# Optimization experiments

Measured on AMD Instinct MI355X. Metric: run time of the kernel, lower is better.

Reference implementation:

```python
import jax, jax.numpy as jnp
import numpy as np

N, E_SC, E_BB = 50000, 600000, 100000
D, ED, REMB, NRES, SBF = 128, 128, 32, 21, 16
PI = 3.14159


def ln(x, g, b):
    m = jnp.mean(x, -1, keepdims=True)
    v = jnp.mean((x - m) ** 2, -1, keepdims=True)
    return (x - m) * jax.lax.rsqrt(v + 1e-5) * g + b


def gcn(x, W, b, src, dst, w):
    # GCNConv: symmetric normalization with unit self-loops and edge weights w.
    n = x.shape[0]
    xw = x @ W
    deg = jax.ops.segment_sum(w, dst, num_segments=n) + 1.0  # +1 self-loop
    dis = jax.lax.rsqrt(jnp.maximum(deg, 1e-6))  # clamp: hat_e.mean can be negative
    norm = dis[src] * w * dis[dst]
    agg = jax.ops.segment_sum(norm[:, None] * xw[src], dst, num_segments=n)
    return agg + (dis * dis)[:, None] * xw + b


def core(V_com, SBF_chi, X_c_alpha, V_c_beta, SBF_phi, SBF_psi, d_sidechain_com, d_min,
         old_chi, old_phi, old_psi, old_cbeta_coords, old_calpha_coords,
         res_table, sc_ln_g, sc_ln_b, sc_W, sc_b, bb_ln_g, bb_ln_b, bb_W, bb_b,
         e_ln_g, e_ln_b, eW1, eb1, eW2, eb2, euW, eub, gW, gb, bgW, bgb,
         iW1, ib1, iW2, ib2, aW, ab, baW, bab, cW, cb, xW, xb,
         residue_idx_i, residue_idx_j, edge_index_sc, edge_index_bb):
    hat_h = ln(jnp.concatenate([V_com, SBF_chi], -1), sc_ln_g, sc_ln_b) @ sc_W + sc_b
    h = ln(jnp.concatenate([X_c_alpha, V_c_beta, SBF_phi, SBF_psi], -1), bb_ln_g, bb_ln_b) @ bb_W + bb_b
    pair = jnp.concatenate([res_table[residue_idx_i], res_table[residue_idx_j]], -1)
    e_in = jnp.concatenate([d_sidechain_com[:, None], d_min[:, None], pair], -1)
    hat_e = jax.nn.relu(ln(e_in, e_ln_g, e_ln_b) @ eW1 + eb1) @ eW2 + eb2
    src, dst = edge_index_sc[0], edge_index_sc[1]
    for _ in range(3):  # num_sidechain_layers
        w = hat_e.mean(-1)
        hat_h = hat_h + jax.nn.relu(gcn(hat_h, gW, gb, src, dst, w))
        hat_e = hat_e + jnp.concatenate([hat_h[src], hat_h[dst]], -1) @ euW + eub
    bsrc, bdst = edge_index_bb[0], edge_index_bb[1]
    ebb = jnp.ones(bsrc.shape[0], hat_h.dtype)
    for _ in range(2):
        m = jax.nn.relu(jnp.concatenate([h, hat_h], -1) @ iW1 + ib1) @ iW2 + ib2
        h = h + jax.nn.relu(gcn(h, bgW, bgb, bsrc, bdst, ebb)) + m
    sc_act = jax.nn.relu(hat_h)
    bb_act = jax.nn.relu(h)
    wrap = lambda a: (a + PI) % (2.0 * PI) - PI
    dchi = (sc_act @ aW + ab)[:, 0]
    chi_new = wrap(old_chi + dchi[None, :])  # [4, N]
    dphi = (bb_act @ baW + bab)[:, 0]
    phi_new = wrap(old_phi + dphi)
    psi_new = wrap(old_psi + dphi)  # same bb_angle_head applied twice in source
    V_cbeta_new = old_cbeta_coords + sc_act @ cW + cb
    X_calpha_new = old_calpha_coords + bb_act @ xW + xb
    return chi_new, phi_new, psi_new, V_cbeta_new, X_calpha_new


def setup_inputs() -> dict:
    key = jax.random.key(0)
    ks = jax.random.split(key, 40)
    rn = lambda i, s: jax.random.normal(ks[i], s, jnp.float32)
    p = lambda i, s: rn(i, s) * 0.05
    return dict(
        V_com=rn(0, (N, 3)), SBF_chi=rn(1, (N, SBF)), X_c_alpha=rn(2, (N, 3)),
        V_c_beta=rn(3, (N, 3)), SBF_phi=rn(4, (N, SBF)), SBF_psi=rn(5, (N, SBF)),
        d_sidechain_com=jax.random.uniform(ks[6], (E_SC,), jnp.float32),
        d_min=jax.random.uniform(ks[7], (E_SC,), jnp.float32),
        old_chi=rn(8, (4, N)), old_phi=rn(9, (N,)), old_psi=rn(10, (N,)),
        old_cbeta_coords=rn(11, (N, 3)), old_calpha_coords=rn(12, (N, 3)),
        res_table=p(13, (NRES, REMB)),
        sc_ln_g=jnp.ones(3 + SBF), sc_ln_b=jnp.zeros(3 + SBF), sc_W=p(14, (3 + SBF, D)), sc_b=jnp.zeros(D),
        bb_ln_g=jnp.ones(6 + 2 * SBF), bb_ln_b=jnp.zeros(6 + 2 * SBF), bb_W=p(15, (6 + 2 * SBF, D)), bb_b=jnp.zeros(D),
        e_ln_g=jnp.ones(2 + 2 * REMB), e_ln_b=jnp.zeros(2 + 2 * REMB),
        eW1=p(16, (2 + 2 * REMB, ED)), eb1=jnp.zeros(ED), eW2=p(17, (ED, ED)), eb2=jnp.zeros(ED),
        euW=p(18, (2 * D, ED)), eub=jnp.zeros(ED),
        gW=p(19, (D, D)), gb=jnp.zeros(D), bgW=p(20, (D, D)), bgb=jnp.zeros(D),
        iW1=p(21, (2 * D, D)), ib1=jnp.zeros(D), iW2=p(22, (D, D)), ib2=jnp.zeros(D),
        aW=p(23, (D, 1)), ab=jnp.zeros(1), baW=p(24, (D, 1)), bab=jnp.zeros(1),
        cW=p(25, (D, 3)), cb=jnp.zeros(3), xW=p(26, (D, 3)), xb=jnp.zeros(3),
        residue_idx_i=jax.random.randint(ks[27], (E_SC,), 0, NRES),
        residue_idx_j=jax.random.randint(ks[28], (E_SC,), 0, NRES),
        edge_index_sc=jax.random.randint(ks[29], (2, E_SC), 0, N),
        edge_index_bb=jax.random.randint(ks[30], (2, E_BB), 0, N),
    )


def reference(V_com, SBF_chi, X_c_alpha, V_c_beta, SBF_phi, SBF_psi, d_sidechain_com, d_min,
              old_chi, old_phi, old_psi, old_cbeta_coords, old_calpha_coords,
              res_table, sc_ln_g, sc_ln_b, sc_W, sc_b, bb_ln_g, bb_ln_b, bb_W, bb_b,
              e_ln_g, e_ln_b, eW1, eb1, eW2, eb2, euW, eub, gW, gb, bgW, bgb,
              iW1, ib1, iW2, ib2, aW, ab, baW, bab, cW, cb, xW, xb,
              residue_idx_i, residue_idx_j, edge_index_sc, edge_index_bb):
    return core(V_com, SBF_chi, X_c_alpha, V_c_beta, SBF_phi, SBF_psi, d_sidechain_com, d_min,
                old_chi, old_phi, old_psi, old_cbeta_coords, old_calpha_coords,
                res_table, sc_ln_g, sc_ln_b, sc_W, sc_b, bb_ln_g, bb_ln_b, bb_W, bb_b,
                e_ln_g, e_ln_b, eW1, eb1, eW2, eb2, euW, eub, gW, gb, bgW, bgb,
                iW1, ib1, iW2, ib2, aW, ab, baW, bab, cW, cb, xW, xb,
                residue_idx_i, residue_idx_j, edge_index_sc, edge_index_bb)
```

## Files before the change

### kernel.cpp

```cpp
#include <hip/hip_runtime.h>
#include <stdint.h>

#define DEVI __device__ __forceinline__

constexpr int N_   = 50000;
constexpr int ESC  = 600000;
constexpr int EBB  = 100000;
constexpr int NRES = 21;
constexpr float PI_F = 3.14159f;

constexpr int RCH = 2048;
constexpr int RBS = (ESC + RCH - 1)/RCH;
constexpr int RBB = (EBB + RCH - 1)/RCH;

typedef __attribute__((ext_vector_type(8))) short short8v;
typedef __attribute__((ext_vector_type(4))) float f32x4;

DEVI float bf2f(unsigned short u){ return __uint_as_float(((unsigned)u)<<16); }
DEVI unsigned short f2bf(float f){
  unsigned x = __float_as_uint(f);
  unsigned r = (x + 0x7FFFu + ((x>>16)&1u))>>16;
  return (unsigned short)r;
}
DEVI float ldin(const void* p, long i, int f32){
// ... 196 lines not shown
  int NB = g? RBB : RBS;
  int* H = hist + (g? (long)RBS*256 : 0);
  int t=threadIdx.x;
  int i0=t, i1=t+256;
  int o0 = (i0<NB)? H[(long)i0*256+d] : 0;
  int o1 = (i1<NB)? H[(long)i1*256+d] : 0;
  sA[i0]=o0; sA[i1]=o1;
  __syncthreads();
  int* a=sA; int* b=sB;
  for(int off=1; off<512; off<<=1){
    b[i0] = a[i0] + ((i0>=off)? a[i0-off]:0);
    b[i1] = a[i1] + ((i1>=off)? a[i1-off]:0);
    __syncthreads();
    int* tmp=a; a=b; b=tmp;
  }
  if(i0<NB) H[(long)i0*256+d] = a[i0]-o0;
  if(i1<NB) H[(long)i1*256+d] = a[i1]-o1;
  if(t==255) tot[(g?256:0)+d] = a[511];
}
__global__ void k_rscanB(const int* tot, int* base){
  __shared__ int sA[256], sB[256];
  int t=threadIdx.x;
  for(int g=0;g<2;g++){
    int o=tot[g*256+t];
    sA[t]=o; __syncthreads();
    int* a=sA; int* b=sB;
    for(int off=1; off<256; off<<=1){
      b[t] = a[t] + ((t>=off)? a[t-off]:0);
      __syncthreads();
      int* tmp=a; a=b; b=tmp;
    }
    base[g*256+t] = a[t]-o;
    __syncthreads();
  }
}
__global__ void k_rscat(int shift, int first,
    const int* kin_sc, const int* srcv_sc, const int2* pin_sc,
    const int* kin_bb, const int* srcv_bb, const int2* pin_bb,
    const int* hist, const int* dbase,
    int* kout_sc, int2* pout_sc, int* kout_bb, int2* pout_bb){
  __shared__ int running[256];
  __shared__ int Hb[256];
  __shared__ int whist[4][256];
  __shared__ int pw[4][256];
  int tid=threadIdx.x, lane=tid&63, w=tid>>6;
  int g = blockIdx.x>=RBS;
  const int* kin  = g? kin_bb : kin_sc;
  const int* srcv = g? srcv_bb: srcv_sc;
  const int2* pin = g? pin_bb : pin_sc;
  int* kout  = g? kout_bb : kout_sc;
  int2* pout = g? pout_bb : pout_sc;
  int E = g? EBB : ESC;
  int b = g? blockIdx.x-RBS : blockIdx.x;
  running[tid]=0;
  Hb[tid]=hist[(long)blockIdx.x*256+tid] + dbase[(g?256:0)+tid];
  int base=b*RCH;
  for(int r=0;r<RCH/256;r++){
    __syncthreads();
    whist[0][tid]=0; whist[1][tid]=0; whist[2][tid]=0; whist[3][tid]=0;
    __syncthreads();
    int idx=base+r*256+tid;
    bool valid = idx<E;
    int key=0, digit=0; int2 pay; pay.x=0; pay.y=0;
    if(valid){
      key=kin[idx];
      digit=(key>>shift)&255;
      if(first){ pay.x=srcv[idx]; pay.y=idx; }
      else pay=pin[idx];
    }
    unsigned long long act=__ballot(valid);
    unsigned long long same=act;
    #pragma unroll
    for(int k=0;k<8;k++){
      unsigned long long m=__ballot(valid && ((digit>>k)&1));
      same &= ((digit>>k)&1)? m : ~m;
    }
    same &= act;
    unsigned long long below=(1ULL<<lane)-1ULL;
    int wrank=__popcll(same & below);
    if(valid && wrank==0) whist[w][digit]=__popcll(same);
    __syncthreads();
    int c0=whist[0][tid], c1=whist[1][tid], c2=whist[2][tid], c3=whist[3][tid];
    pw[0][tid]=0; pw[1][tid]=c0; pw[2][tid]=c0+c1; pw[3][tid]=c0+c1+c2;
    __syncthreads();
    if(valid){
      int pos=Hb[digit]+running[digit]+pw[w][digit]+wrank;
      kout[pos]=key; pout[pos]=pay;
    }
    __syncthreads();
    running[tid]+=c0+c1+c2+c3;
  }
}
__global__ void k_bounds(const int* dstS_sc, const int* dstS_bb, int* rp_sc, int* rp_bb){
  long i=(long)blockIdx.x*blockDim.x+threadIdx.x;
  if(i<=ESC){
    int cur = (i<ESC)? dstS_sc[i] : N_;
    int prev= (i>0)? dstS_sc[i-1] : -1;
    for(int d=prev+1; d<=cur; d++) rp_sc[d]=(int)i;
  } else if(i <= (long)ESC+1+EBB){
    long j=i-(ESC+1);
    int cur = (j<EBB)? dstS_bb[j] : N_;
    int prev= (j>0)? dstS_bb[j-1] : -1;
    for(int d=prev+1; d<=cur; d++) rp_bb[d]=(int)j;
  }
}
__global__ void k_degb(const int* rp, float* disb){
  int n=blockIdx.x*blockDim.x+threadIdx.x;
  if(n<N_) disb[n]=rsqrtf(1.f+(float)(rp[n+1]-rp[n]));
}

constexpr int WBG = (ESC + 63)/64;
__global__ __launch_bounds__(256,4) void k_w0(const void* dsc, const void* dmin,
    const int* ri_, const int* rj_, const int* flag, const float* dvf,
    const float* P, const float* sp, const float* qp, float* we){
  int wv=threadIdx.x>>6, lane=threadIdx.x&63;
  int g=lane>>4, l=lane&15;
  long ebase=(long)blockIdx.x*64 + wv*16 + g*4;
  int f32=*flag;
  int j0=l*8;
  float4 A0=*(const float4*)&dvf[j0],     A1=*(const float4*)&dvf[j0+4];
  float4 C0=*(const float4*)&dvf[128+j0], C1=*(const float4*)&dvf[128+j0+4];
  float4 G0=*(const float4*)&dvf[256+j0], G1=*(const float4*)&dvf[256+j0+4];
  float4 B0=*(const float4*)&dvf[384+j0], B1=*(const float4*)&dvf[384+j0+4];
  float4 V0=*(const float4*)&dvf[512+j0], V1=*(const float4*)&dvf[512+j0+4];
  float eb2=dvf[640];
  #pragma unroll
  for(int k=0;k<4;k++){
    long e=ebase+k;
    bool val = e<ESC;
    long ee = val? e : 0;
    float d1=ldin(dsc,ee,f32), d2=ldin(dmin,ee,f32);
    int c=ri_[ee]*NRES+rj_[ee];
    float m=(d1+d2+sp[c])*(1.f/66.f);
    float ms=(d1*d1+d2*d2+qp[c])*(1.f/66.f);
    float istd=rsqrtf(fmaxf(ms-m*m,0.f)+1e-5f);
    float nmi=-m*istd;
    float4 P0=*(const float4*)&P[(long)c*128+j0];
    float4 P1=*(const float4*)&P[(long)c*128+j0+4];
    float acc=0.f, t, hid;
    t=fmaf(d1,A0.x,fmaf(d2,C0.x,P0.x)); hid=fmaf(istd,t,fmaf(nmi,G0.x,B0.x)); acc=fmaf(fmaxf(hid,0.f),V0.x,acc);
    t=fmaf(d1,A0.y,fmaf(d2,C0.y,P0.y)); hid=fmaf(istd,t,fmaf(nmi,G0.y,B0.y)); acc=fmaf(fmaxf(hid,0.f),V0.y,acc);
    t=fmaf(d1,A0.z,fmaf(d2,C0.z,P0.z)); hid=fmaf(istd,t,fmaf(nmi,G0.z,B0.z)); acc=fmaf(fmaxf(hid,0.f),V0.z,acc);
    t=fmaf(d1,A0.w,fmaf(d2,C0.w,P0.w)); hid=fmaf(istd,t,fmaf(nmi,G0.w,B0.w)); acc=fmaf(fmaxf(hid,0.f),V0.w,acc);
    t=fmaf(d1,A1.x,fmaf(d2,C1.x,P1.x)); hid=fmaf(istd,t,fmaf(nmi,G1.x,B1.x)); acc=fmaf(fmaxf(hid,0.f),V1.x,acc);
    t=fmaf(d1,A1.y,fmaf(d2,C1.y,P1.y)); hid=fmaf(istd,t,fmaf(nmi,G1.y,B1.y)); acc=fmaf(fmaxf(hid,0.f),V1.y,acc);
    t=fmaf(d1,A1.z,fmaf(d2,C1.z,P1.z)); hid=fmaf(istd,t,fmaf(nmi,G1.z,B1.z)); acc=fmaf(fmaxf(hid,0.f),V1.z,acc);
    t=fmaf(d1,A1.w,fmaf(d2,C1.w,P1.w)); hid=fmaf(istd,t,fmaf(nmi,G1.w,B1.w)); acc=fmaf(fmaxf(hid,0.f),V1.w,acc);
    #pragma unroll
    for(int msk=1;msk<16;msk<<=1) acc+=__shfl_xor(acc,msk,64);
    if(l==0 && val) we[e]=acc+eb2;
  }
}

__global__ void k_deg(const int* rp, const int2* se, const float* we_edge,
                      const float* an, const float* bn, const float* dv,
                      float* we_csr, float* dis, int layer){
  int n=blockIdx.x*blockDim.x+threadIdx.x;
  if(n>=N_) return;
  int e0=rp[n], e1=rp[n+1];
  float s=1.f;
  if(layer==0){
    for(int p=e0;p<e1;p++){ float ww=we_edge[se[p].y]; we_csr[p]=ww; s+=ww; }
  } else {
    float add_n = bn[n] + dv[897];
    for(int p=e0;p<e1;p++){
      float ww=we_csr[p] + an[se[p].x] + add_n;
      we_csr[p]=ww; s+=ww;
    }
  }
  dis[n]=rsqrtf(fmaxf(s,1e-6f));
}
__global__ void k_norm(const int2* se, const float* we_csr, const float* dis, float* wn){
  int p=blockIdx.x*blockDim.x+threadIdx.x;
  if(p<ESC) wn[p]=dis[se[p].x]*we_csr[p];
}

DEVI f32x4 MFMA(short8v a, short8v b, f32x4 c){
  return __builtin_amdgcn_mfma_f32_16x16x32_bf16(a,b,c,0,0,0);
}
DEVI void cvt8(float4 a0, float4 a1, short8v& hi, short8v& lo){
  float av[8]={a0.x,a0.y,a0.z,a0.w,a1.x,a1.y,a1.z,a1.w};
  union{short8v v; unsigned short u[8];} H,L;
  #pragma unroll
  for(int i=0;i<8;i++){
    unsigned short h=f2bf(av[i]);
    float r=av[i]-bf2f(h);
    H.u[i]=h; L.u[i]=f2bf(r);
  }
  hi=H.v; lo=L.v;
}
DEVI short8v cvt8hi(float4 a0, float4 a1){
  union{short8v v; unsigned short u[8];} H;
  H.u[0]=f2bf(a0.x); H.u[1]=f2bf(a0.y); H.u[2]=f2bf(a0.z); H.u[3]=f2bf(a0.w);
  H.u[4]=f2bf(a1.x); H.u[5]=f2bf(a1.y); H.u[6]=f2bf(a1.z); H.u[7]=f2bf(a1.w);
  return H.v;
}

template<int KT, int LDA>
DEVI void mgemm_body(int bid, const float* A1, const float* A2,
    const unsigned short* Whi, const unsigned short* Wlo,
    const float* bias, float* C, int relu, int accum, int M){
  const int lane = threadIdx.x & 63;
  const int wid  = threadIdx.x >> 6;
  const int r0   = bid*64 + wid*16;
  const int mrow = lane & 15;
  const int kg   = lane >> 4;
  long arow = (long)min(r0 + mrow, M-1);
  f32x4 acc[8];
  #pragma unroll
  for(int t=0;t<8;t++) acc[t]=(f32x4){0.f,0.f,0.f,0.f};

  #pragma unroll
  for(int kt=0; kt<KT; kt++){
    const float* A = (KT==8 && kt>=4) ? A2 : A1;
    int kb = (kt&3)*32 + kg*8;
    float4 a0 = *(const float4*)&A[arow*LDA + kb];
    float4 a1 = *(const float4*)&A[arow*LDA + kb + 4];
    short8v ah, al; cvt8(a0,a1,ah,al);
    #pragma unroll
    for(int nt=0;nt<8;nt++){
      long off = (((long)kt*8+nt)*64 + lane)*8;
      short8v wh = *(const short8v*)&Whi[off];
      short8v wl = *(const short8v*)&Wlo[off];
      acc[nt] = MFMA(ah, wh, acc[nt]);
      acc[nt] = MFMA(al, wh, acc[nt]);
      acc[nt] = MFMA(ah, wl, acc[nt]);
      acc[nt] = MFMA(al, wl, acc[nt]);
    }
  }

  #pragma unroll
  for(int nt=0;nt<8;nt++){
    int col = nt*16 + mrow;
    float bj = bias ? bias[col] : 0.f;
    #pragma unroll
    for(int r=0;r<4;r++){
      int row = r0 + kg*4 + r;
      if(row >= M) continue;
      long idx = (long)row*128 + col;
      float v = acc[nt][r] + bj;
      if(relu) v = fmaxf(v,0.f);
      if(accum) v += C[idx];
      C[idx] = v;
    }
  }
}

template<int KT, int LDA>
__global__ __launch_bounds__(256,4) void k_mgemm(const float* A1, const float* A2,
    const unsigned short* Whi, const unsigned short* Wlo,
    const float* bias, float* C, int relu, int accum, int M){
  mgemm_body<KT,LDA>(blockIdx.x, A1, A2, Whi, Wlo, bias, C, relu, accum, M);
}

__global__ __launch_bounds__(256,4) void k_mfeat(const float* xn_sc, const float* xn_bb,
    const unsigned short* schi, const unsigned short* sclo,
    const unsigned short* bbhi, const unsigned short* bblo,
    const float* w, float* hat_h, float* hbuf, int M){
  int GBl=(M+63)/64;
  if((int)blockIdx.x < GBl)
    mgemm_body<1,32>(blockIdx.x, xn_sc, nullptr, schi, sclo, w+OW_SC_B, hat_h, 0,0,M);
  else
    mgemm_body<2,64>(blockIdx.x-GBl, xn_bb, nullptr, bbhi, bblo, w+OW_BB_B, hbuf, 0,0,M);
}

__global__ __launch_bounds__(256,4) void k_mbb(const float* h, const float* hh,
    const unsigned short* W1hi,
    const unsigned short* W2hi,
    const unsigned short* W3hi,
    const float* b1, const float* b2,
    unsigned short* xwout, unsigned short* mout, int M){
  __shared__ unsigned short hids[64*136];
  const int lane = threadIdx.x & 63;
  const int wid  = threadIdx.x >> 6;
  const int r0   = blockIdx.x*64 + wid*16;
  const int mrow = lane & 15;
  const int kg   = lane >> 4;
  long arow = (long)min(r0 + mrow, M-1);
  f32x4 acc1[8], acc2[8];
  #pragma unroll
  for(int t=0;t<8;t++){ acc1[t]=(f32x4){0,0,0,0}; acc2[t]=(f32x4){0,0,0,0}; }

  #pragma unroll
  for(int kt=0; kt<8; kt++){
    const float* A = (kt>=4) ? hh : h;
    int kb = (kt&3)*32 + kg*8;
    float4 a0 = *(const float4*)&A[arow*128 + kb];
    float4 a1 = *(const float4*)&A[arow*128 + kb + 4];
    short8v ah = cvt8hi(a0,a1);
    #pragma unroll
    for(int nt=0;nt<8;nt++){
      long off = (((long)kt*8+nt)*64 + lane)*8;
      acc1[nt] = MFMA(ah, *(const short8v*)&W1hi[off], acc1[nt]);
    }
    if(kt<4){
      #pragma unroll
      for(int nt=0;nt<8;nt++){
        long off = (((long)kt*8+nt)*64 + lane)*8;
        acc2[nt] = MFMA(ah, *(const short8v*)&W2hi[off], acc2[nt]);
      }
    }
  }

  #pragma unroll
  for(int nt=0;nt<8;nt++){
    int col = nt*16 + mrow;
    float bj = b1[col];
    #pragma unroll
    for(int r=0;r<4;r++){
      int rloc = wid*16 + kg*4 + r;
      int row = r0 + kg*4 + r;
      hids[rloc*136 + col] = f2bf(fmaxf(acc1[nt][r] + bj, 0.f));
      if(row < M) xwout[(long)row*128 + col] = f2bf(acc2[nt][r]);
    }
  }
  __syncthreads();

  f32x4 acc3[8];
  #pragma unroll
  for(int t=0;t<8;t++) acc3[t]=(f32x4){0,0,0,0};
  int rloc = wid*16 + mrow;
  #pragma unroll
  for(int kt=0; kt<4; kt++){
    int kb = kt*32 + kg*8;
    short8v ah = *(const short8v*)&hids[rloc*136 + kb];
    #pragma unroll
    for(int nt=0;nt<8;nt++){
      long off = (((long)kt*8+nt)*64 + lane)*8;
      acc3[nt] = MFMA(ah, *(const short8v*)&W3hi[off], acc3[nt]);
    }
  }
  #pragma unroll
  for(int nt=0;nt<8;nt++){
    int col = nt*16 + mrow;
    float bj = b2[col];
    #pragma unroll
    for(int r=0;r<4;r++){
      int row = r0 + kg*4 + r;
      if(row < M) mout[(long)row*128 + col] = f2bf(acc3[nt][r] + bj);
    }
  }
}

__global__ void k_agg_sc(const int* rp, const int2* se, const float* wn,
                         const float* dis, const float* xw, const float* w,
                         float* hat_h, const float* dv, float* an, float* bn, int withdot){
  int wv=threadIdx.x>>6, lane=threadIdx.x&63;
  int n=blockIdx.x*4+wv;
  int g=lane>>4, l=lane&15, d0=l*8;
  float disn=dis[n];
  float4 aA={0,0,0,0}, aB={0,0,0,0}, cA={0,0,0,0}, cB={0,0,0,0};
  int e0=rp[n], e1=rp[n+1];
  int p=e0+g;
  for(; p+4<e1; p+=8){
    int s0=se[p].x, s1=se[p+4].x;
    float nw0=wn[p], nw1=wn[p+4];
    float4 xa0=*(const float4*)&xw[(long)s0*128+d0];
    float4 xb0=*(const float4*)&xw[(long)s0*128+d0+4];
    float4 xa1=*(const float4*)&xw[(long)s1*128+d0];
    float4 xb1=*(const float4*)&xw[(long)s1*128+d0+4];
    aA.x+=nw0*xa0.x; aA.y+=nw0*xa0.y; aA.z+=nw0*xa0.z; aA.w+=nw0*xa0.w;
    aB.x+=nw0*xb0.x; aB.y+=nw0*xb0.y; aB.z+=nw0*xb0.z; aB.w+=nw0*xb0.w;
    cA.x+=nw1*xa1.x; cA.y+=nw1*xa1.y; cA.z+=nw1*xa1.z; cA.w+=nw1*xa1.w;
    cB.x+=nw1*xb1.x; cB.y+=nw1*xb1.y; cB.z+=nw1*xb1.z; cB.w+=nw1*xb1.w;
  }
  if(p<e1){
    int s0=se[p].x;
    float nw0=wn[p];
    float4 xa0=*(const float4*)&xw[(long)s0*128+d0];
    float4 xb0=*(const float4*)&xw[(long)s0*128+d0+4];
    aA.x+=nw0*xa0.x; aA.y+=nw0*xa0.y; aA.z+=nw0*xa0.z; aA.w+=nw0*xa0.w;
    aB.x+=nw0*xb0.x; aB.y+=nw0*xb0.y; aB.z+=nw0*xb0.z; aB.w+=nw0*xb0.w;
  }
  aA.x+=cA.x; aA.y+=cA.y; aA.z+=cA.z; aA.w+=cA.w;
  aB.x+=cB.x; aB.y+=cB.y; aB.z+=cB.z; aB.w+=cB.w;
  #pragma unroll
  for(int m=16;m<64;m<<=1){
    aA.x+=__shfl_xor(aA.x,m,64); aA.y+=__shfl_xor(aA.y,m,64);
    aA.z+=__shfl_xor(aA.z,m,64); aA.w+=__shfl_xor(aA.w,m,64);
    aB.x+=__shfl_xor(aB.x,m,64); aB.y+=__shfl_xor(aB.y,m,64);
    aB.z+=__shfl_xor(aB.z,m,64); aB.w+=__shfl_xor(aB.w,m,64);
  }
  float d2=disn*disn;
  float4 xsA=*(const float4*)&xw[(long)n*128+d0];
  float4 xsB=*(const float4*)&xw[(long)n*128+d0+4];
  float4 gbA=*(const float4*)&w[OW_GB+d0];
  float4 gbB=*(const float4*)&w[OW_GB+d0+4];
  float4 hoA=*(const float4*)&hat_h[(long)n*128+d0];
  float4 hoB=*(const float4*)&hat_h[(long)n*128+d0+4];
  float4 hA, hB;
  hA.x=hoA.x+fmaxf(aA.x*disn+d2*xsA.x+gbA.x,0.f);
  hA.y=hoA.y+fmaxf(aA.y*disn+d2*xsA.y+gbA.y,0.f);
  hA.z=hoA.z+fmaxf(aA.z*disn+d2*xsA.z+gbA.z,0.f);
  hA.w=hoA.w+fmaxf(aA.w*disn+d2*xsA.w+gbA.w,0.f);
  hB.x=hoB.x+fmaxf(aB.x*disn+d2*xsB.x+gbB.x,0.f);
  hB.y=hoB.y+fmaxf(aB.y*disn+d2*xsB.y+gbB.y,0.f);
  hB.z=hoB.z+fmaxf(aB.z*disn+d2*xsB.z+gbB.z,0.f);
  hB.w=hoB.w+fmaxf(aB.w*disn+d2*xsB.w+gbB.w,0.f);
  if(g==0){
    *(float4*)&hat_h[(long)n*128+d0]=hA;
    *(float4*)&hat_h[(long)n*128+d0+4]=hB;
  }
  if(withdot){
    float4 usA=*(const float4*)&dv[640+d0], usB=*(const float4*)&dv[640+d0+4];
    float4 udA=*(const float4*)&dv[768+d0], udB=*(const float4*)&dv[768+d0+4];
    float a = hA.x*usA.x+hA.y*usA.y+hA.z*usA.z+hA.w*usA.w
            + hB.x*usB.x+hB.y*usB.y+hB.z*usB.z+hB.w*usB.w;
    float b = hA.x*udA.x+hA.y*udA.y+hA.z*udA.z+hA.w*udA.w
            + hB.x*udB.x+hB.y*udB.y+hB.z*udB.z+hB.w*udB.w;
    #pragma unroll
    for(int m=1;m<16;m<<=1){ a+=__shfl_xor(a,m,64); b+=__shfl_xor(b,m,64); }
    if(lane==0){ an[n]=a; bn[n]=b; }
  }
}

DEVI void bf8ld(const unsigned short* p, float4& lo, float4& hi){
  union{short8v v; unsigned short u[8];} t;
  t.v = *(const short8v*)p;
  lo.x=bf2f(t.u[0]); lo.y=bf2f(t.u[1]); lo.z=bf2f(t.u[2]); lo.w=bf2f(t.u[3]);
  hi.x=bf2f(t.u[4]); hi.y=bf2f(t.u[5]); hi.z=bf2f(t.u[6]); hi.w=bf2f(t.u[7]);
}

__global__ void k_agg_bb(const int* rp, const int2* se, const float* disb,
                         const unsigned short* xw, const unsigned short* mbuf,
                         const float* w, float* h){
  int wv=threadIdx.x>>6, lane=threadIdx.x&63;
  int n=blockIdx.x*4+wv;
  int g=lane>>4, l=lane&15, d0=l*8;
  int e0=rp[n], e1=rp[n+1];
  float disn=disb[n];
  float4 aA={0,0,0,0}, aB={0,0,0,0}, cA={0,0,0,0}, cB={0,0,0,0};
  int p=e0+g;
  for(; p+4<e1; p+=8){
    int s0=se[p].x, s1=se[p+4].x;
    float nw0=disb[s0], nw1=disb[s1];
    float4 xa0,xb0,xa1,xb1;
    bf8ld(&xw[(long)s0*128+d0], xa0, xb0);
    bf8ld(&xw[(long)s1*128+d0], xa1, xb1);
    aA.x+=nw0*xa0.x; aA.y+=nw0*xa0.y; aA.z+=nw0*xa0.z; aA.w+=nw0*xa0.w;
    aB.x+=nw0*xb0.x; aB.y+=nw0*xb0.y; aB.z+=nw0*xb0.z; aB.w+=nw0*xb0.w;
    cA.x+=nw1*xa1.x; cA.y+=nw1*xa1.y; cA.z+=nw1*xa1.z; cA.w+=nw1*xa1.w;
    cB.x+=nw1*xb1.x; cB.y+=nw1*xb1.y; cB.z+=nw1*xb1.z; cB.w+=nw1*xb1.w;
  }
  if(p<e1){
    int s0=se[p].x;
    float nw0=disb[s0];
    float4 xa0,xb0;
    bf8ld(&xw[(long)s0*128+d0], xa0, xb0);
    aA.x+=nw0*xa0.x; aA.y+=nw0*xa0.y; aA.z+=nw0*xa0.z; aA.w+=nw0*xa0.w;
    aB.x+=nw0*xb0.x; aB.y+=nw0*xb0.y; aB.z+=nw0*xb0.z; aB.w+=nw0*xb0.w;
  }
  aA.x+=cA.x; aA.y+=cA.y; aA.z+=cA.z; aA.w+=cA.w;
  aB.x+=cB.x; aB.y+=cB.y; aB.z+=cB.z; aB.w+=cB.w;
  #pragma unroll
  for(int m=16;m<64;m<<=1){
    aA.x+=__shfl_xor(aA.x,m,64); aA.y+=__shfl_xor(aA.y,m,64);
    aA.z+=__shfl_xor(aA.z,m,64); aA.w+=__shfl_xor(aA.w,m,64);
    aB.x+=__shfl_xor(aB.x,m,64); aB.y+=__shfl_xor(aB.y,m,64);
    aB.z+=__shfl_xor(aB.z,m,64); aB.w+=__shfl_xor(aB.w,m,64);
  }
  if(g==0){
    float d2=disn*disn;
    float4 xsA,xsB,mA,mB;
    bf8ld(&xw[(long)n*128+d0], xsA, xsB);
    bf8ld(&mbuf[(long)n*128+d0], mA, mB);
    float4 gbA=*(const float4*)&w[OW_BGB+d0];
    float4 gbB=*(const float4*)&w[OW_BGB+d0+4];
    float4 hA=*(float4*)&h[(long)n*128+d0];
    float4 hB=*(float4*)&h[(long)n*128+d0+4];
    hA.x+=fmaxf(aA.x*disn+d2*xsA.x+gbA.x,0.f)+mA.x;
    hA.y+=fmaxf(aA.y*disn+d2*xsA.y+gbA.y,0.f)+mA.y;
    hA.z+=fmaxf(aA.z*disn+d2*xsA.z+gbA.z,0.f)+mA.z;
    hA.w+=fmaxf(aA.w*disn+d2*xsA.w+gbA.w,0.f)+mA.w;
    hB.x+=fmaxf(aB.x*disn+d2*xsB.x+gbB.x,0.f)+mB.x;
    hB.y+=fmaxf(aB.y*disn+d2*xsB.y+gbB.y,0.f)+mB.y;
    hB.z+=fmaxf(aB.z*disn+d2*xsB.z+gbB.z,0.f)+mB.z;
    hB.w+=fmaxf(aB.w*disn+d2*xsB.w+gbB.w,0.f)+mB.w;
    *(float4*)&h[(long)n*128+d0]=hA;
    *(float4*)&h[(long)n*128+d0+4]=hB;
  }
}

__global__ void k_heads(const float* hat_h, const float* h, const float* w,
                        const void* old_chi, const void* old_phi, const void* old_psi,
                        const void* old_cb, const void* old_ca, const int* flag, void* out){
  int wv=threadIdx.x>>6, lane=threadIdx.x&63;
  int n=blockIdx.x*4+wv;
  int f32=*flag;
  float s0=fmaxf(hat_h[(long)n*128+lane],0.f), s1=fmaxf(hat_h[(long)n*128+64+lane],0.f);
  float b0=fmaxf(h[(long)n*128+lane],0.f),    b1=fmaxf(h[(long)n*128+64+lane],0.f);
  float r[8];
  r[0]=s0*w[OW_AW+lane]+s1*w[OW_AW+64+lane];
  r[1]=s0*w[OW_CW+lane*3+0]+s1*w[OW_CW+(64+lane)*3+0];
  r[2]=s0*w[OW_CW+lane*3+1]+s1*w[OW_CW+(64+lane)*3+1];
  r[3]=s0*w[OW_CW+lane*3+2]+s1*w[OW_CW+(64+lane)*3+2];
  r[4]=b0*w[OW_BAW+lane]+b1*w[OW_BAW+64+lane];
  r[5]=b0*w[OW_XW+lane*3+0]+b1*w[OW_XW+(64+lane)*3+0];
  r[6]=b0*w[OW_XW+lane*3+1]+b1*w[OW_XW+(64+lane)*3+1];
  r[7]=b0*w[OW_XW+lane*3+2]+b1*w[OW_XW+(64+lane)*3+2];
  for(int m=1;m<64;m<<=1){
    #pragma unroll
    for(int t=0;t<8;t++) r[t]+=__shfl_xor(r[t],m,64);
  }
  if(lane==0){
    float dchi=r[0]+w[OW_AB];
    for(int k=0;k<4;k++)
      stout(out,(long)k*N_+n, wrapf(ldin(old_chi,(long)k*N_+n,f32)+dchi), f32);
    float dphi=r[4]+w[OW_BAB];
    stout(out,(long)4*N_+n, wrapf(ldin(old_phi,n,f32)+dphi), f32);
    stout(out,(long)5*N_+n, wrapf(ldin(old_psi,n,f32)+dphi), f32);
    for(int t=0;t<3;t++){
      stout(out,(long)6*N_+(long)n*3+t, ldin(old_cb,(long)n*3+t,f32)+r[1+t]+w[OW_CB+t], f32);
      stout(out,(long)9*N_+(long)n*3+t, ldin(old_ca,(long)n*3+t,f32)+r[5+t]+w[OW_XB+t], f32);
    }
  }
}

extern "C" void kernel_launch(void* const* d_in, const int* in_sizes, int n_in,
                              void* d_out, int out_size, void* d_ws, size_t ws_size,
                              hipStream_t stream) {
  (void)in_sizes; (void)n_in; (void)out_size; (void)ws_size;

  char* p=(char*)d_ws;
  auto alloc=[&](size_t bytes)->void*{ void* r=(void*)p; p+=((bytes+255)&~(size_t)255); return r; };
  int*   flag   =(int*)  alloc(16);
  float* warena =(float*)alloc((size_t)OW_TOT*4);
  float* dv     =(float*)alloc(1024*4);
  float* dvf    =(float*)alloc(1024*4);
  float* P      =(float*)alloc((size_t)441*128*4);
  float* sp     =(float*)alloc(441*4);
  float* qp     =(float*)alloc(441*4);
  float* hat_h  =(float*)alloc((size_t)N_*128*4);
  float* hbuf   =(float*)alloc((size_t)N_*128*4);
  float* bufX   =(float*)alloc((size_t)N_*128*4);
  unsigned short* bufXb=(unsigned short*)alloc((size_t)N_*128*2);
  unsigned short* bufMb=(unsigned short*)alloc((size_t)N_*128*2);
  float* xn_sc  =(float*)alloc((size_t)N_*32*4);
  float* xn_bb  =(float*)alloc((size_t)N_*64*4);
  float* we     =(float*)alloc((size_t)ESC*4);
  float* we_csr =(float*)alloc((size_t)ESC*4);
  float* wn     =(float*)alloc((size_t)ESC*4);
  float* an     =(float*)alloc((size_t)N_*4);
  float* bn     =(float*)alloc((size_t)N_*4);
  float* dis    =(float*)alloc((size_t)N_*4);
  float* disb   =(float*)alloc((size_t)N_*4);
  int* rp_sc    =(int*)  alloc((size_t)(N_+1)*4);
  int* rp_bb    =(int*)  alloc((size_t)(N_+1)*4);
  int*  key1_sc =(int*)  alloc((size_t)ESC*4);
  int2* pay1_sc =(int2*) alloc((size_t)ESC*8);
  int*  dstS_sc =(int*)  alloc((size_t)ESC*4);
  int2* csr_se_sc=(int2*)alloc((size_t)ESC*8);
  int*  key1_bb =(int*)  alloc((size_t)EBB*4);
  int2* pay1_bb =(int2*) alloc((size_t)EBB*8);
  int*  dstS_bb =(int*)  alloc((size_t)EBB*4);
  int2* csr_se_bb=(int2*)alloc((size_t)EBB*8);
  int*  hist    =(int*)  alloc((size_t)(RBS+RBB)*256*4);
  int*  tot     =(int*)  alloc(512*4);
  int*  dbase   =(int*)  alloc(512*4);
  unsigned short* wfg_hi =(unsigned short*)alloc(2048*8*2);
  unsigned short* wfg_lo =(unsigned short*)alloc(2048*8*2);
  unsigned short* wfbg_hi=(unsigned short*)alloc(2048*8*2);
  unsigned short* wfi2_hi=(unsigned short*)alloc(2048*8*2);
  unsigned short* wfi1_hi=(unsigned short*)alloc(4096*8*2);
  unsigned short* wfsc_hi=(unsigned short*)alloc(512*8*2);
  unsigned short* wfsc_lo=(unsigned short*)alloc(512*8*2);
  unsigned short* wfbb_hi=(unsigned short*)alloc(1024*8*2);
  unsigned short* wfbb_lo=(unsigned short*)alloc(1024*8*2);

  const int* src_sc=(const int*)d_in[48];
  const int* dst_sc=src_sc+ESC;
  const int* src_bb=(const int*)d_in[49];
  const int* dst_bb=src_bb+EBB;

  k_detect<<<1,1,0,stream>>>(d_in[0], flag);

  CvtArgs ca;
  {
    int map[29]={14,15,16,17,18,19,20,21,22,23,24,25,30,31,32,33,34,35,36,37,
                 38,39,40,41,42,43,44,45,13};
    for(int i=0;i<29;i++) ca.src[i]=d_in[map[i]];
  }
  k_cvtw<<<(OW_TOT+255)/256,256,0,stream>>>(ca, flag, warena);

  k_prep<<<PB_LN,256,0,stream>>>(warena, flag,
      wfg_hi,wfg_lo, wfbg_hi, wfi2_hi, wfi1_hi,
      wfsc_hi,wfsc_lo, wfbb_hi,wfbb_lo,
      d_in[26], d_in[27], d_in[28], d_in[29], dv, dvf, P, sp, qp,
      d_in[0], d_in[1], d_in[2], d_in[3], d_in[4], d_in[5], xn_sc, xn_bb);

  k_rhist<<<RBS+RBB,256,0,stream>>>(dst_sc, dst_bb, 0, hist);
  k_rscanA<<<512,256,0,stream>>>(hist, tot);
  k_rscanB<<<1,256,0,stream>>>(tot, dbase);
  k_rscat<<<RBS+RBB,256,0,stream>>>(0, 1, dst_sc, src_sc, (const int2*)nullptr,
                                    dst_bb, src_bb, (const int2*)nullptr, hist, dbase,
                                    key1_sc, pay1_sc, key1_bb, pay1_bb);
  k_rhist<<<RBS+RBB,256,0,stream>>>(key1_sc, key1_bb, 8, hist);
  k_rscanA<<<512,256,0,stream>>>(hist, tot);
  k_rscanB<<<1,256,0,stream>>>(tot, dbase);
  k_rscat<<<RBS+RBB,256,0,stream>>>(8, 0, key1_sc, (const int*)nullptr, pay1_sc,
                                    key1_bb, (const int*)nullptr, pay1_bb, hist, dbase,
                                    dstS_sc, csr_se_sc, dstS_bb, csr_se_bb);
  k_bounds<<<(int)(((long)ESC+1+EBB+1+255)/256),256,0,stream>>>(dstS_sc, dstS_bb, rp_sc, rp_bb);
  k_degb<<<(N_+255)/256,256,0,stream>>>(rp_bb, disb);

  const int GB = (N_+63)/64;
  k_mfeat<<<2*GB,256,0,stream>>>(xn_sc, xn_bb, wfsc_hi, wfsc_lo, wfbb_hi, wfbb_lo,
                                 warena, hat_h, hbuf, N_);

  k_w0<<<WBG,256,0,stream>>>(d_in[6],d_in[7],(const int*)d_in[46],(const int*)d_in[47],
                             flag,dvf,P,sp,qp,we);

  const int DB = (N_+255)/256;
  const int NB = (ESC+255)/256;
  for(int l=0;l<3;l++){
    k_deg<<<DB,256,0,stream>>>(rp_sc, csr_se_sc, we, an, bn, dv, we_csr, dis, l);
    k_norm<<<NB,256,0,stream>>>(csr_se_sc, we_csr, dis, wn);
    k_mgemm<4,128><<<GB,256,0,stream>>>(hat_h, nullptr, wfg_hi, wfg_lo, nullptr, bufX, 0, 0, N_);
    k_agg_sc<<<N_/4,256,0,stream>>>(rp_sc,csr_se_sc,wn,dis,bufX,warena,hat_h,dv,an,bn,(l<2)?1:0);
  }

  for(int l=0;l<2;l++){
    k_mbb<<<GB,256,0,stream>>>(hbuf, hat_h, wfi1_hi, wfbg_hi, wfi2_hi,
                               warena+OW_IB1, warena+OW_IB2, bufXb, bufMb, N_);
    k_agg_bb<<<N_/4,256,0,stream>>>(rp_bb,csr_se_bb,disb,bufXb,bufMb,warena,hbuf);
  }

  k_heads<<<N_/4,256,0,stream>>>(hat_h,hbuf,warena,
                                 d_in[8],d_in[9],d_in[10],d_in[11],d_in[12],flag,d_out);
}
```

Measured before the change: 610.7 us.

## Fuse degree computation into GCN GEMM launch and widen per-lane aggregation slices

The per-node degree/normalization kernel and the independent sidechain GEMM now run as one grid, with extra blocks past the GEMM blocks doing the degree work, so the two overlap and one launch per layer is saved. Separately, both aggregation kernels now give each lane 16 features instead of 8 and process 8 edges in parallel per wave instead of 4, with loads unrolled to 4 float4 per row. This trades more registers per lane for more memory-level parallelism in the edge gather and fewer shuffle reduction steps. Mixing GEMM and scalar blocks in one grid can unbalance scheduling, and the GEMM's launch bounds now also cover the degree blocks.

Result: slower. 691.6 us (+13.2%).

```diff
diff --git a/kernel.cpp b/kernel.cpp
--- a/kernel.cpp
+++ b/kernel.cpp
@@ -372,29 +372,6 @@
   }
 }
 
-__global__ void k_deg(const int* rp, const int2* se, const float* we_edge,
-                      const float* an, const float* bn, const float* dv,
-                      float* we_csr, float* dis, int layer){
-  int n=blockIdx.x*blockDim.x+threadIdx.x;
-  if(n>=N_) return;
-  int e0=rp[n], e1=rp[n+1];
-  float s=1.f;
-  if(layer==0){
-    for(int p=e0;p<e1;p++){ float ww=we_edge[se[p].y]; we_csr[p]=ww; s+=ww; }
-  } else {
-    float add_n = bn[n] + dv[897];
-    for(int p=e0;p<e1;p++){
-      float ww=we_csr[p] + an[se[p].x] + add_n;
-      we_csr[p]=ww; s+=ww;
-    }
-  }
-  dis[n]=rsqrtf(fmaxf(s,1e-6f));
-}
-__global__ void k_norm(const int2* se, const float* we_csr, const float* dis, float* wn){
-  int p=blockIdx.x*blockDim.x+threadIdx.x;
-  if(p<ESC) wn[p]=dis[se[p].x]*we_csr[p];
-}
-
 DEVI f32x4 MFMA(short8v a, short8v b, f32x4 c){
   return __builtin_amdgcn_mfma_f32_16x16x32_bf16(a,b,c,0,0,0);
 }
@@ -466,11 +443,35 @@
   }
 }
 
-template<int KT, int LDA>
-__global__ __launch_bounds__(256,4) void k_mgemm(const float* A1, const float* A2,
-    const unsigned short* Whi, const unsigned short* Wlo,
-    const float* bias, float* C, int relu, int accum, int M){
-  mgemm_body<KT,LDA>(blockIdx.x, A1, A2, Whi, Wlo, bias, C, relu, accum, M);
+__global__ __launch_bounds__(256,4) void k_gemmdeg(const float* hat_h,
+    const unsigned short* Whi, const unsigned short* Wlo, float* C, int M,
+    const int* rp, const int2* se, const float* we_edge,
+    const float* an, const float* bn, const float* dv,
+    float* we_csr, float* dis, int layer){
+  int GBl=(M+63)/64;
+  if((int)blockIdx.x < GBl){
+    mgemm_body<4,128>(blockIdx.x, hat_h, nullptr, Whi, Wlo, nullptr, C, 0, 0, M);
+  } else {
+    int n=(blockIdx.x-GBl)*256+threadIdx.x;
+    if(n>=N_) return;
+    int e0=rp[n], e1=rp[n+1];
+    float s=1.f;
+    if(layer==0){
+      for(int p=e0;p<e1;p++){ float ww=we_edge[se[p].y]; we_csr[p]=ww; s+=ww; }
+    } else {
+      float add_n = bn[n] + dv[897];
+      for(int p=e0;p<e1;p++){
+        float ww=we_csr[p] + an[se[p].x] + add_n;
+        we_csr[p]=ww; s+=ww;
+      }
+    }
+    dis[n]=rsqrtf(fmaxf(s,1e-6f));
+  }
+}
+
+__global__ void k_norm(const int2* se, const float* we_csr, const float* dis, float* wn){
+  int p=blockIdx.x*blockDim.x+threadIdx.x;
+  if(p<ESC) wn[p]=dis[se[p].x]*we_csr[p];
 }
 
 __global__ __launch_bounds__(256,4) void k_mfeat(const float* xn_sc, const float* xn_bb,
@@ -567,69 +568,83 @@
                          float* hat_h, const float* dv, float* an, float* bn, int withdot){
   int wv=threadIdx.x>>6, lane=threadIdx.x&63;
   int n=blockIdx.x*4+wv;
-  int g=lane>>4, l=lane&15, d0=l*8;
+  int g=lane>>3, l=lane&7, d0=l*16;
   float disn=dis[n];
-  float4 aA={0,0,0,0}, aB={0,0,0,0}, cA={0,0,0,0}, cB={0,0,0,0};
+  float4 a0={0,0,0,0},a1={0,0,0,0},a2={0,0,0,0},a3={0,0,0,0};
+  float4 c0={0,0,0,0},c1={0,0,0,0},c2={0,0,0,0},c3={0,0,0,0};
   int e0=rp[n], e1=rp[n+1];
   int p=e0+g;
-  for(; p+4<e1; p+=8){
-    int s0=se[p].x, s1=se[p+4].x;
-    float nw0=wn[p], nw1=wn[p+4];
-    float4 xa0=*(const float4*)&xw[(long)s0*128+d0];
-    float4 xb0=*(const float4*)&xw[(long)s0*128+d0+4];
-    float4 xa1=*(const float4*)&xw[(long)s1*128+d0];
-    float4 xb1=*(const float4*)&xw[(long)s1*128+d0+4];
-    aA.x+=nw0*xa0.x; aA.y+=nw0*xa0.y; aA.z+=nw0*xa0.z; aA.w+=nw0*xa0.w;
-    aB.x+=nw0*xb0.x; aB.y+=nw0*xb0.y; aB.z+=nw0*xb0.z; aB.w+=nw0*xb0.w;
-    cA.x+=nw1*xa1.x; cA.y+=nw1*xa1.y; cA.z+=nw1*xa1.z; cA.w+=nw1*xa1.w;
-    cB.x+=nw1*xb1.x; cB.y+=nw1*xb1.y; cB.z+=nw1*xb1.z; cB.w+=nw1*xb1.w;
+  for(; p+8<e1; p+=16){
+    int s0=se[p].x, s1=se[p+8].x;
+    float nw0=wn[p], nw1=wn[p+8];
+    const float4* r0=(const float4*)&xw[(long)s0*128+d0];
+    const float4* r1=(const float4*)&xw[(long)s1*128+d0];
+    float4 x0=r0[0],x1=r0[1],x2=r0[2],x3=r0[3];
+    float4 y0=r1[0],y1=r1[1],y2=r1[2],y3=r1[3];
+    a0.x+=nw0*x0.x; a0.y+=nw0*x0.y; a0.z+=nw0*x0.z; a0.w+=nw0*x0.w;
+    a1.x+=nw0*x1.x; a1.y+=nw0*x1.y; a1.z+=nw0*x1.z; a1.w+=nw0*x1.w;
+    a2.x+=nw0*x2.x; a2.y+=nw0*x2.y; a2.z+=nw0*x2.z; a2.w+=nw0*x2.w;
+    a3.x+=nw0*x3.x; a3.y+=nw0*x3.y; a3.z+=nw0*x3.z; a3.w+=nw0*x3.w;
+    c0.x+=nw1*y0.x; c0.y+=nw1*y0.y; c0.z+=nw1*y0.z; c0.w+=nw1*y0.w;
+    c1.x+=nw1*y1.x; c1.y+=nw1*y1.y; c1.z+=nw1*y1.z; c1.w+=nw1*y1.w;
+    c2.x+=nw1*y2.x; c2.y+=nw1*y2.y; c2.z+=nw1*y2.z; c2.w+=nw1*y2.w;
+    c3.x+=nw1*y3.x; c3.y+=nw1*y3.y; c3.z+=nw1*y3.z; c3.w+=nw1*y3.w;
   }
   if(p<e1){
     int s0=se[p].x;
     float nw0=wn[p];
-    float4 xa0=*(const float4*)&xw[(long)s0*128+d0];
-    float4 xb0=*(const float4*)&xw[(long)s0*128+d0+4];
-    aA.x+=nw0*xa0.x; aA.y+=nw0*xa0.y; aA.z+=nw0*xa0.z; aA.w+=nw0*xa0.w;
-    aB.x+=nw0*xb0.x; aB.y+=nw0*xb0.y; aB.z+=nw0*xb0.z; aB.w+=nw0*xb0.w;
-  }
-  aA.x+=cA.x; aA.y+=cA.y; aA.z+=cA.z; aA.w+=cA.w;
-  aB.x+=cB.x; aB.y+=cB.y; aB.z+=cB.z; aB.w+=cB.w;
-  #pragma unroll
-  for(int m=16;m<64;m<<=1){
-    aA.x+=__shfl_xor(aA.x,m,64); aA.y+=__shfl_xor(aA.y,m,64);
-    aA.z+=__shfl_xor(aA.z,m,64); aA.w+=__shfl_xor(aA.w,m,64);
-    aB.x+=__shfl_xor(aB.x,m,64); aB.y+=__shfl_xor(aB.y,m,64);
-    aB.z+=__shfl_xor(aB.z,m,64); aB.w+=__shfl_xor(aB.w,m,64);
+    const float4* r0=(const float4*)&xw[(long)s0*128+d0];
+    float4 x0=r0[0],x1=r0[1],x2=r0[2],x3=r0[3];
+    a0.x+=nw0*x0.x; a0.y+=nw0*x0.y; a0.z+=nw0*x0.z; a0.w+=nw0*x0.w;
+    a1.x+=nw0*x1.x; a1.y+=nw0*x1.y; a1.z+=nw0*x1.z; a1.w+=nw0*x1.w;
+    a2.x+=nw0*x2.x; a2.y+=nw0*x2.y; a2.z+=nw0*x2.z; a2.w+=nw0*x2.w;
+    a3.x+=nw0*x3.x; a3.y+=nw0*x3.y; a3.z+=nw0*x3.z; a3.w+=nw0*x3.w;
+  }
+  a0.x+=c0.x; a0.y+=c0.y; a0.z+=c0.z; a0.w+=c0.w;
+  a1.x+=c1.x; a1.y+=c1.y; a1.z+=c1.z; a1.w+=c1.w;
+  a2.x+=c2.x; a2.y+=c2.y; a2.z+=c2.z; a2.w+=c2.w;
+  a3.x+=c3.x; a3.y+=c3.y; a3.z+=c3.z; a3.w+=c3.w;
+  #pragma unroll
+  for(int m=8;m<64;m<<=1){
+    a0.x+=__shfl_xor(a0.x,m,64); a0.y+=__shfl_xor(a0.y,m,64);
+    a0.z+=__shfl_xor(a0.z,m,64); a0.w+=__shfl_xor(a0.w,m,64);
+    a1.x+=__shfl_xor(a1.x,m,64); a1.y+=__shfl_xor(a1.y,m,64);
+    a1.z+=__shfl_xor(a1.z,m,64); a1.w+=__shfl_xor(a1.w,m,64);
+    a2.x+=__shfl_xor(a2.x,m,64); a2.y+=__shfl_xor(a2.y,m,64);
+    a2.z+=__shfl_xor(a2.z,m,64); a2.w+=__shfl_xor(a2.w,m,64);
+    a3.x+=__shfl_xor(a3.x,m,64); a3.y+=__shfl_xor(a3.y,m,64);
+    a3.z+=__shfl_xor(a3.z,m,64); a3.w+=__shfl_xor(a3.w,m,64);
   }
   float d2=disn*disn;
-  float4 xsA=*(const float4*)&xw[(long)n*128+d0];
-  float4 xsB=*(const float4*)&xw[(long)n*128+d0+4];
-  float4 gbA=*(const float4*)&w[OW_GB+d0];
-  float4 gbB=*(const float4*)&w[OW_GB+d0+4];
-  float4 hoA=*(const float4*)&hat_h[(long)n*128+d0];
-  float4 hoB=*(const float4*)&hat_h[(long)n*128+d0+4];
-  float4 hA, hB;
-  hA.x=hoA.x+fmaxf(aA.x*disn+d2*xsA.x+gbA.x,0.f);
-  hA.y=hoA.y+fmaxf(aA.y*disn+d2*xsA.y+gbA.y,0.f);
-  hA.z=hoA.z+fmaxf(aA.z*disn+d2*xsA.z+gbA.z,0.f);
-  hA.w=hoA.w+fmaxf(aA.w*disn+d2*xsA.w+gbA.w,0.f);
-  hB.x=hoB.x+fmaxf(aB.x*disn+d2*xsB.x+gbB.x,0.f);
-  hB.y=hoB.y+fmaxf(aB.y*disn+d2*xsB.y+gbB.y,0.f);
-  hB.z=hoB.z+fmaxf(aB.z*disn+d2*xsB.z+gbB.z,0.f);
-  hB.w=hoB.w+fmaxf(aB.w*disn+d2*xsB.w+gbB.w,0.f);
+  const float4* xs=(const float4*)&xw[(long)n*128+d0];
+  const float4* gb=(const float4*)&w[OW_GB+d0];
+  float4* hp=(float4*)&hat_h[(long)n*128+d0];
+  float4 hv[4];
+  float4 av[4]={a0,a1,a2,a3};
+  #pragma unroll
+  for(int q=0;q<4;q++){
+    float4 xq=xs[q], gq=gb[q], hq=hp[q];
+    hv[q].x=hq.x+fmaxf(av[q].x*disn+d2*xq.x+gq.x,0.f);
+    hv[q].y=hq.y+fmaxf(av[q].y*disn+d2*xq.y+gq.y,0.f);
+    hv[q].z=hq.z+fmaxf(av[q].z*disn+d2*xq.z+gq.z,0.f);
+    hv[q].w=hq.w+fmaxf(av[q].w*disn+d2*xq.w+gq.w,0.f);
+  }
   if(g==0){
-    *(float4*)&hat_h[(long)n*128+d0]=hA;
-    *(float4*)&hat_h[(long)n*128+d0+4]=hB;
+    #pragma unroll
+    for(int q=0;q<4;q++) hp[q]=hv[q];
   }
   if(withdot){
-    float4 usA=*(const float4*)&dv[640+d0], usB=*(const float4*)&dv[640+d0+4];
-    float4 udA=*(const float4*)&dv[768+d0], udB=*(const float4*)&dv[768+d0+4];
-    float a = hA.x*usA.x+hA.y*usA.y+hA.z*usA.z+hA.w*usA.w
-            + hB.x*usB.x+hB.y*usB.y+hB.z*usB.z+hB.w*usB.w;
-    float b = hA.x*udA.x+hA.y*udA.y+hA.z*udA.z+hA.w*udA.w
-            + hB.x*udB.x+hB.y*udB.y+hB.z*udB.z+hB.w*udB.w;
-    #pragma unroll
-    for(int m=1;m<16;m<<=1){ a+=__shfl_xor(a,m,64); b+=__shfl_xor(b,m,64); }
+    const float4* us=(const float4*)&dv[640+d0];
+    const float4* ud=(const float4*)&dv[768+d0];
+    float a=0.f, b=0.f;
+    #pragma unroll
+    for(int q=0;q<4;q++){
+      float4 u=us[q], v=ud[q];
+      a += hv[q].x*u.x+hv[q].y*u.y+hv[q].z*u.z+hv[q].w*u.w;
+      b += hv[q].x*v.x+hv[q].y*v.y+hv[q].z*v.z+hv[q].w*v.w;
+    }
+    #pragma unroll
+    for(int m=1;m<8;m<<=1){ a+=__shfl_xor(a,m,64); b+=__shfl_xor(b,m,64); }
     if(lane==0){ an[n]=a; bn[n]=b; }
   }
 }
@@ -646,58 +661,74 @@
                          const float* w, float* h){
   int wv=threadIdx.x>>6, lane=threadIdx.x&63;
   int n=blockIdx.x*4+wv;
-  int g=lane>>4, l=lane&15, d0=l*8;
+  int g=lane>>3, l=lane&7, d0=l*16;
   int e0=rp[n], e1=rp[n+1];
   float disn=disb[n];
-  float4 aA={0,0,0,0}, aB={0,0,0,0}, cA={0,0,0,0}, cB={0,0,0,0};
+  float4 a0={0,0,0,0},a1={0,0,0,0},a2={0,0,0,0},a3={0,0,0,0};
+  float4 c0={0,0,0,0},c1={0,0,0,0},c2={0,0,0,0},c3={0,0,0,0};
   int p=e0+g;
-  for(; p+4<e1; p+=8){
-    int s0=se[p].x, s1=se[p+4].x;
+  for(; p+8<e1; p+=16){
+    int s0=se[p].x, s1=se[p+8].x;
     float nw0=disb[s0], nw1=disb[s1];
-    float4 xa0,xb0,xa1,xb1;
-    bf8ld(&xw[(long)s0*128+d0], xa0, xb0);
-    bf8ld(&xw[(long)s1*128+d0], xa1, xb1);
-    aA.x+=nw0*xa0.x; aA.y+=nw0*xa0.y; aA.z+=nw0*xa0.z; aA.w+=nw0*xa0.w;
-    aB.x+=nw0*xb0.x; aB.y+=nw0*xb0.y; aB.z+=nw0*xb0.z; aB.w+=nw0*xb0.w;
-    cA.x+=nw1*xa1.x; cA.y+=nw1*xa1.y; cA.z+=nw1*xa1.z; cA.w+=nw1*xa1.w;
-    cB.x+=nw1*xb1.x; cB.y+=nw1*xb1.y; cB.z+=nw1*xb1.z; cB.w+=nw1*xb1.w;
+    float4 x0,x1,x2,x3,y0,y1,y2,y3;
+    bf8ld(&xw[(long)s0*128+d0], x0, x1);
+    bf8ld(&xw[(long)s0*128+d0+8], x2, x3);
+    bf8ld(&xw[(long)s1*128+d0], y0, y1);
+    bf8ld(&xw[(long)s1*128+d0+8], y2, y3);
+    a0.x+=nw0*x0.x; a0.y+=nw0*x0.y; a0.z+=nw0*x0.z; a0.w+=nw0*x0.w;
+    a1.x+=nw0*x1.x; a1.y+=nw0*x1.y; a1.z+=nw0*x1.z; a1.w+=nw0*x1.w;
+    a2.x+=nw0*x2.x; a2.y+=nw0*x2.y; a2.z+=nw0*x2.z; a2.w+=nw0*x2.w;
+    a3.x+=nw0*x3.x; a3.y+=nw0*x3.y; a3.z+=nw0*x3.z; a3.w+=nw0*x3.w;
+    c0.x+=nw1*y0.x; c0.y+=nw1*y0.y; c0.z+=nw1*y0.z; c0.w+=nw1*y0.w;
+    c1.x+=nw1*y1.x; c1.y+=nw1*y1.y; c1.z+=nw1*y1.z; c1.w+=nw1*y1.w;
+    c2.x+=nw1*y2.x; c2.y+=nw1*y2.y; c2.z+=nw1*y2.z; c2.w+=nw1*y2.w;
+    c3.x+=nw1*y3.x; c3.y+=nw1*y3.y; c3.z+=nw1*y3.z; c3.w+=nw1*y3.w;
   }
   if(p<e1){
     int s0=se[p].x;
     float nw0=disb[s0];
-    float4 xa0,xb0;
-    bf8ld(&xw[(long)s0*128+d0], xa0, xb0);
-    aA.x+=nw0*xa0.x; aA.y+=nw0*xa0.y; aA.z+=nw0*xa0.z; aA.w+=nw0*xa0.w;
-    aB.x+=nw0*xb0.x; aB.y+=nw0*xb0.y; aB.z+=nw0*xb0.z; aB.w+=nw0*xb0.w;
-  }
-  aA.x+=cA.x; aA.y+=cA.y; aA.z+=cA.z; aA.w+=cA.w;
-  aB.x+=cB.x; aB.y+=cB.y; aB.z+=cB.z; aB.w+=cB.w;
-  #pragma unroll
-  for(int m=16;m<64;m<<=1){
-    aA.x+=__shfl_xor(aA.x,m,64); aA.y+=__shfl_xor(aA.y,m,64);
-    aA.z+=__shfl_xor(aA.z,m,64); aA.w+=__shfl_xor(aA.w,m,64);
-    aB.x+=__shfl_xor(aB.x,m,64); aB.y+=__shfl_xor(aB.y,m,64);
-    aB.z+=__shfl_xor(aB.z,m,64); aB.w+=__shfl_xor(aB.w,m,64);
+    float4 x0,x1,x2,x3;
+    bf8ld(&xw[(long)s0*128+d0], x0, x1);
+    bf8ld(&xw[(long)s0*128+d0+8], x2, x3);
+    a0.x+=nw0*x0.x; a0.y+=nw0*x0.y; a0.z+=nw0*x0.z; a0.w+=nw0*x0.w;
+    a1.x+=nw0*x1.x; a1.y+=nw0*x1.y; a1.z+=nw0*x1.z; a1.w+=nw0*x1.w;
+    a2.x+=nw0*x2.x; a2.y+=nw0*x2.y; a2.z+=nw0*x2.z; a2.w+=nw0*x2.w;
+    a3.x+=nw0*x3.x; a3.y+=nw0*x3.y; a3.z+=nw0*x3.z; a3.w+=nw0*x3.w;
+  }
+  a0.x+=c0.x; a0.y+=c0.y; a0.z+=c0.z; a0.w+=c0.w;
+  a1.x+=c1.x; a1.y+=c1.y; a1.z+=c1.z; a1.w+=c1.w;
+  a2.x+=c2.x; a2.y+=c2.y; a2.z+=c2.z; a2.w+=c2.w;
+  a3.x+=c3.x; a3.y+=c3.y; a3.z+=c3.z; a3.w+=c3.w;
+  #pragma unroll
+  for(int m=8;m<64;m<<=1){
+    a0.x+=__shfl_xor(a0.x,m,64); a0.y+=__shfl_xor(a0.y,m,64);
+    a0.z+=__shfl_xor(a0.z,m,64); a0.w+=__shfl_xor(a0.w,m,64);
+    a1.x+=__shfl_xor(a1.x,m,64); a1.y+=__shfl_xor(a1.y,m,64);
+    a1.z+=__shfl_xor(a1.z,m,64); a1.w+=__shfl_xor(a1.w,m,64);
+    a2.x+=__shfl_xor(a2.x,m,64); a2.y+=__shfl_xor(a2.y,m,64);
+    a2.z+=__shfl_xor(a2.z,m,64); a2.w+=__shfl_xor(a2.w,m,64);
+    a3.x+=__shfl_xor(a3.x,m,64); a3.y+=__shfl_xor(a3.y,m,64);
+    a3.z+=__shfl_xor(a3.z,m,64); a3.w+=__shfl_xor(a3.w,m,64);
   }
   if(g==0){
     float d2=disn*disn;
-    float4 xsA,xsB,mA,mB;
-    bf8ld(&xw[(long)n*128+d0], xsA, xsB);
-    bf8ld(&mbuf[(long)n*128+d0], mA, mB);
-    float4 gbA=*(const float4*)&w[OW_BGB+d0];
-    float4 gbB=*(const float4*)&w[OW_BGB+d0+4];
-    float4 hA=*(float4*)&h[(long)n*128+d0];
-    float4 hB=*(float4*)&h[(long)n*128+d0+4];
-    hA.x+=fmaxf(aA.x*disn+d2*xsA.x+gbA.x,0.f)+mA.x;
-    hA.y+=fmaxf(aA.y*disn+d2*xsA.y+gbA.y,0.f)+mA.y;
-    hA.z+=fmaxf(aA.z*disn+d2*xsA.z+gbA.z,0.f)+mA.z;
-    hA.w+=fmaxf(aA.w*disn+d2*xsA.w+gbA.w,0.f)+mA.w;
-    hB.x+=fmaxf(aB.x*disn+d2*xsB.x+gbB.x,0.f)+mB.x;
-    hB.y+=fmaxf(aB.y*disn+d2*xsB.y+gbB.y,0.f)+mB.y;
-    hB.z+=fmaxf(aB.z*disn+d2*xsB.z+gbB.z,0.f)+mB.z;
-    hB.w+=fmaxf(aB.w*disn+d2*xsB.w+gbB.w,0.f)+mB.w;
-    *(float4*)&h[(long)n*128+d0]=hA;
-    *(float4*)&h[(long)n*128+d0+4]=hB;
+    float4 xs[4], mm[4];
+    bf8ld(&xw[(long)n*128+d0], xs[0], xs[1]);
+    bf8ld(&xw[(long)n*128+d0+8], xs[2], xs[3]);
+    bf8ld(&mbuf[(long)n*128+d0], mm[0], mm[1]);
+    bf8ld(&mbuf[(long)n*128+d0+8], mm[2], mm[3]);
+    const float4* gb=(const float4*)&w[OW_BGB+d0];
+    float4* hp=(float4*)&h[(long)n*128+d0];
+    float4 av[4]={a0,a1,a2,a3};
+    #pragma unroll
+    for(int q=0;q<4;q++){
+      float4 hq=hp[q], gq=gb[q];
+      hq.x+=fmaxf(av[q].x*disn+d2*xs[q].x+gq.x,0.f)+mm[q].x;
+      hq.y+=fmaxf(av[q].y*disn+d2*xs[q].y+gq.y,0.f)+mm[q].y;
+      hq.z+=fmaxf(av[q].z*disn+d2*xs[q].z+gq.z,0.f)+mm[q].z;
+      hq.w+=fmaxf(av[q].w*disn+d2*xs[q].w+gq.w,0.f)+mm[q].w;
+      hp[q]=hq;
+    }
   }
 }
 
@@ -833,9 +864,9 @@
   const int DB = (N_+255)/256;
   const int NB = (ESC+255)/256;
   for(int l=0;l<3;l++){
-    k_deg<<<DB,256,0,stream>>>(rp_sc, csr_se_sc, we, an, bn, dv, we_csr, dis, l);
+    k_gemmdeg<<<GB+DB,256,0,stream>>>(hat_h, wfg_hi, wfg_lo, bufX, N_,
+                                      rp_sc, csr_se_sc, we, an, bn, dv, we_csr, dis, l);
     k_norm<<<NB,256,0,stream>>>(csr_se_sc, we_csr, dis, wn);
-    k_mgemm<4,128><<<GB,256,0,stream>>>(hat_h, nullptr, wfg_hi, wfg_lo, nullptr, bufX, 0, 0, N_);
     k_agg_sc<<<N_/4,256,0,stream>>>(rp_sc,csr_se_sc,wn,dis,bufX,warena,hat_h,dv,an,bn,(l<2)?1:0);
   }
 
```
